# Optimization experiments

Measured on AMD Instinct MI355X. Metric: run time of the kernel, lower is better.

The kernel has to match this reference:

```python
import jax, jax.numpy as jnp
import numpy as np

INF = 1e38  # matches torch source constant


def setup_inputs() -> dict:
    key = jax.random.key(0)
    k1, k2, k3 = jax.random.split(key, 3)
    B, N, D = 16, 2048, 512
    query = jax.random.normal(k1, (B, N, D), dtype=jnp.float32)
    # nn.Linear(dims, dims, bias=False): weight [out, in] = [D, D]
    W_in = jax.random.normal(k2, (D, D), dtype=jnp.float32) * (1.0 / np.sqrt(D))
    # nn.Linear(2*dims, dims, bias=False): weight [D, 2D]
    W_out = jax.random.normal(k3, (D, 2 * D), dtype=jnp.float32) * (1.0 / np.sqrt(2 * D))
    return {"query": query, "W_in": W_in, "W_out": W_out}


def reference(query, W_in, W_out):
    B, N, D = query.shape
    # linear_in: y = x @ W^T
    q = jnp.einsum("bnd,ed->bne", query, W_in)  # [B, N, D]
    # full QK^T scores
    scores = jnp.einsum("bnd,bmd->bnm", q, q)  # [B, N, N]
    # torch: scores[:, triu_mask] = -INF  -> mask upper triangle INCLUDING diagonal
    mask = jnp.triu(jnp.ones((N, N), dtype=bool))
    scores = jnp.where(mask, -INF, scores)
    weights = jax.nn.softmax(scores, axis=-1)
    # row 0 is all -INF -> softmax gives uniform; torch zeroes it explicitly
    weights = weights.at[:, 0, :].set(0.0)
    mix = jnp.einsum("bnm,bmd->bnd", weights, q)  # [B, N, D]
    combined = jnp.concatenate([mix, q], axis=-1)  # [B, N, 2D]
    # linear_out (no activation since activation=None)
    output = jnp.einsum("bnc,dc->bnd", combined, W_out)  # [B, N, D]
    return output
```

## Files before the change

### kernel.cpp

```cpp
#include <hip/hip_runtime.h>

typedef _Float16 f16;
typedef _Float16 half8 __attribute__((ext_vector_type(8)));
typedef _Float16 half4 __attribute__((ext_vector_type(4)));
typedef float floatx4 __attribute__((ext_vector_type(4)));

#define MFMA16(a, b, c) __builtin_amdgcn_mfma_f32_16x16x32_f16(a, b, c, 0, 0, 0)

#define PHASE_WAIT_4()  do { asm volatile("s_waitcnt vmcnt(4)" ::: "memory"); \
    __builtin_amdgcn_sched_barrier(0); __builtin_amdgcn_s_barrier(); } while (0)
#define PHASE_WAIT_0()  do { asm volatile("s_waitcnt vmcnt(0)" ::: "memory"); \
    __builtin_amdgcn_sched_barrier(0); __builtin_amdgcn_s_barrier(); } while (0)

__device__ __forceinline__ void gload16(const void* g, void* l) {
    __builtin_amdgcn_global_load_lds((const __attribute__((address_space(1))) void*)g,
                                     (__attribute__((address_space(3))) void*)l, 16, 0, 0);
}


__global__ __launch_bounds__(256) void k_cvt(const float* __restrict__ query,
                                             const float* __restrict__ Wi,
                                             const float* __restrict__ Wo,
                                             f16* __restrict__ q16,
                                             f16* __restrict__ W16)
{
    int i = blockIdx.x * 256 + threadIdx.x;
    const float4* src;
    f16* dst;
    if (i < 4194304) { src = (const float4*)query + i; dst = q16 + (size_t)i * 4; }
    else if (i < 4259840) { int j = i - 4194304; src = (const float4*)Wi + j; dst = W16 + (size_t)j * 4; }
    else { int j = i - 4259840; src = (const float4*)Wo + j; dst = W16 + 262144 + (size_t)j * 4; }
    float4 v = *src;
    half4 h = {(f16)v.x, (f16)v.y, (f16)v.z, (f16)v.w};
    *reinterpret_cast<half4*>(dst) = h;
}

__global__ __launch_bounds__(512, 4) void k_qin(const f16* __restrict__ q16,
                                                const f16* __restrict__ W16,
                                                f16* __restrict__ comb,
                                                f16* __restrict__ qT)
{
    __shared__ char sm[65536];
    const int tid = threadIdx.x, lane = tid & 63, w = tid >> 6;
    const int l15 = lane & 15, quad = lane >> 4;
    const int id = blockIdx.x, xcd = id & 7, u = id >> 3;
    const int mbase = (xcd * 32 + (u >> 2)) * 128;
    const int nbase = (u & 3) * 128;
    const int wm = (w & 1) * 64, wn = (w >> 1) * 32;
    const int ia = (w & 1) * 4, jb = (w >> 1) * 2;

    floatx4 acc[4][2];
#pragma unroll
    for (int i = 0; i < 4; ++i)
#pragma unroll
        for (int j = 0; j < 2; ++j) acc[i][j] = (floatx4)0.f;

    auto STAGE = [&](int k0, int bsel) {
        f16* At = (f16*)(sm + bsel * 32768);
        f16* Bt = At + 8192;
#pragma unroll
        for (int jr = 0; jr < 2; ++jr) {
            int bi = jr * 8 + w, i2 = bi >> 1, s = bi & 1;
            gload16(q16 + (size_t)(mbase + i2 * 16 + l15) * 512 + k0 + s * 32 + quad * 8, At + bi * 512);
            gload16(W16 + (size_t)(nbase + i2 * 16 + l15) * 512 + k0 + s * 32 + quad * 8, Bt + bi * 512);
        }
    };

    STAGE(0, 0);
    STAGE(64, 1);
    for (int it = 0; it < 8; ++it) {
        const int cur = it & 1;
        if (it < 7) PHASE_WAIT_4(); else PHASE_WAIT_0();
        f16* At = (f16*)(sm + cur * 32768);
        f16* Bt = At + 8192;
#pragma unroll
        for (int s = 0; s < 2; ++s) {
            half8 a[4], bf[2];
#pragma unroll
            for (int i = 0; i < 4; ++i)
                a[i] = *reinterpret_cast<half8*>(At + ((ia + i) * 2 + s) * 512 + lane * 8);
#pragma unroll
            for (int j = 0; j < 2; ++j)
                bf[j] = *reinterpret_cast<half8*>(Bt + ((jb + j) * 2 + s) * 512 + lane * 8);
#pragma unroll
            for (int i = 0; i < 4; ++i)
#pragma unroll
                for (int j = 0; j < 2; ++j)
                    acc[i][j] = MFMA16(a[i], bf[j], acc[i][j]);
        }
        __builtin_amdgcn_s_barrier();
        if (it + 2 < 8) STAGE((it + 2) * 64, cur);
    }
    const int bb = mbase >> 11, tb = mbase & 2047;
    f16* ct = (f16*)sm;
#pragma unroll
    for (int i = 0; i < 4; ++i)
#pragma unroll
        for (int j = 0; j < 2; ++j)
#pragma unroll
            for (int r = 0; r < 4; ++r)
                ct[(wm + i * 16 + quad * 4 + r) * 136 + wn + j * 16 + l15] = (f16)acc[i][j][r];
    __syncthreads();
#pragma unroll
    for (int it = 0; it < 4; ++it) {
        int c = it * 512 + tid, r = c >> 4, c8 = (c & 15) << 3;
        *reinterpret_cast<half8*>(comb + (size_t)(mbase + r) * 1024 + 512 + nbase + c8) =
            *reinterpret_cast<half8*>(ct + r * 136 + c8);
    }
    __syncthreads();
#pragma unroll
    for (int i = 0; i < 4; ++i)
#pragma unroll
        for (int j = 0; j < 2; ++j) {
            half4 h = {(f16)acc[i][j][0], (f16)acc[i][j][1], (f16)acc[i][j][2], (f16)acc[i][j][3]};
            *reinterpret_cast<half4*>(ct + (wn + j * 16 + l15) * 136 + wm + i * 16 + quad * 4) = h;
        }
    __syncthreads();
#pragma unroll
    for (int it = 0; it < 4; ++it) {
        int c = it * 512 + tid, dd = c >> 4, tc = (c & 15) << 3;
        *reinterpret_cast<half8*>(qT + ((size_t)bb * 512 + nbase + dd) * 2048 + tb + tc) =
            *reinterpret_cast<half8*>(ct + dd * 136 + tc);
    }
}

__global__ __launch_bounds__(512, 4) void k_sgemmsm(const f16* __restrict__ comb,
                                                    f16* __restrict__ Pd,
                                                    float* __restrict__ Mt,
                                                    float* __restrict__ Lt)
{
    __shared__ char sm[65536];
    const int tid = threadIdx.x, lane = tid & 63, w = tid >> 6;
    const int l15 = lane & 15, quad = lane >> 4;
    const int wm = (w & 1) * 64, wn = (w >> 1) * 32;
    const int ia = (w & 1) * 4, jb = (w >> 1) * 2;

    const int bhalf = (blockIdx.y >= 136) ? 1 : 0;
    int bx = blockIdx.y - bhalf * 136, mt = 0;
    while ((mt + 1) * (mt + 2) / 2 <= bx) ++mt;
    const int nt = bx - mt * (mt + 1) / 2;
    const int b = blockIdx.x + bhalf * 8;
    const f16* qa = comb + ((size_t)b * 2048 + mt * 128) * 1024 + 512;
    const f16* qb = comb + ((size_t)b * 2048 + nt * 128) * 1024 + 512;

    floatx4 acc[4][2];
#pragma unroll
    for (int i = 0; i < 4; ++i)
#pragma unroll
        for (int j = 0; j < 2; ++j) acc[i][j] = (floatx4)0.f;

    auto STAGE = [&](int k0, int bsel) {
        f16* At = (f16*)(sm + bsel * 32768);
        f16* Bt = At + 8192;
#pragma unroll
        for (int jr = 0; jr < 2; ++jr) {
            int bi = jr * 8 + w, i2 = bi >> 1, s = bi & 1;
            gload16(qa + (size_t)(i2 * 16 + l15) * 1024 + k0 + s * 32 + quad * 8, At + bi * 512);
            gload16(qb + (size_t)(i2 * 16 + l15) * 1024 + k0 + s * 32 + quad * 8, Bt + bi * 512);
        }
    };

    STAGE(0, 0);
    STAGE(64, 1);
    for (int it = 0; it < 8; ++it) {
        const int cur = it & 1;
        if (it < 7) PHASE_WAIT_4(); else PHASE_WAIT_0();
        f16* At = (f16*)(sm + cur * 32768);
        f16* Bt = At + 8192;
#pragma unroll
        for (int s = 0; s < 2; ++s) {
            half8 a[4], bf[2];
#pragma unroll
            for (int i = 0; i < 4; ++i)
                a[i] = *reinterpret_cast<half8*>(At + ((ia + i) * 2 + s) * 512 + lane * 8);
#pragma unroll
            for (int j = 0; j < 2; ++j)
                bf[j] = *reinterpret_cast<half8*>(Bt + ((jb + j) * 2 + s) * 512 + lane * 8);
#pragma unroll
            for (int i = 0; i < 4; ++i)
#pragma unroll
                for (int j = 0; j < 2; ++j)
                    acc[i][j] = MFMA16(a[i], bf[j], acc[i][j]);
        }
        __builtin_amdgcn_s_barrier();
        if (it + 2 < 8) STAGE((it + 2) * 64, cur);
    }

    const bool diag = (nt == mt);
    f16* ct = (f16*)sm;
    float* redm = (float*)(sm + 34816);
    float* reds = (float*)(sm + 36864);
    const int hb = w & 1;

    float wmax[4][4];
#pragma unroll
    for (int i = 0; i < 4; ++i)
#pragma unroll
        for (int r = 0; r < 4; ++r) {
            const int rowl = wm + i * 16 + quad * 4 + r;
            float mm = -1e38f;
#pragma unroll
            for (int j = 0; j < 2; ++j) {
                float v = acc[i][j][r];
                if (diag && (wn + j * 16 + l15) >= rowl) v = -1e38f;
                mm = fmaxf(mm, v);
            }
            mm = fmaxf(mm, __shfl_xor(mm, 1));
            mm = fmaxf(mm, __shfl_xor(mm, 2));
            mm = fmaxf(mm, __shfl_xor(mm, 4));
            mm = fmaxf(mm, __shfl_xor(mm, 8));
            wmax[i][r] = mm;
        }
    if (l15 == 0)
#pragma unroll
        for (int i = 0; i < 4; ++i)
#pragma unroll
            for (int r = 0; r < 4; ++r)
                redm[w * 64 + i * 16 + quad * 4 + r] = wmax[i][r];
    __syncthreads();

#pragma unroll
    for (int i = 0; i < 4; ++i)
#pragma unroll
        for (int r = 0; r < 4; ++r) {
            const int idx = i * 16 + quad * 4 + r;
            const int rowl = wm + idx;
            const float m = fmaxf(fmaxf(redm[hb * 64 + idx], redm[(hb + 2) * 64 + idx]),
                                  fmaxf(redm[(hb + 4) * 64 + idx], redm[(hb + 6) * 64 + idx]));
            float ssum = 0.f;
#pragma unroll
            for (int j = 0; j < 2; ++j) {
                const int col = wn + j * 16 + l15;
                const bool valid = !diag || (col < rowl);
                float e = valid ? __expf(acc[i][j][r] - m) : 0.f;
                ssum += e;
                ct[rowl * 136 + col] = (f16)e;
            }
            ssum += __shfl_xor(ssum, 1);
            ssum += __shfl_xor(ssum, 2);
            ssum += __shfl_xor(ssum, 4);
            ssum += __shfl_xor(ssum, 8);
            wmax[i][r] = ssum;
        }
    if (l15 == 0)
#pragma unroll
        for (int i = 0; i < 4; ++i)
#pragma unroll
            for (int r = 0; r < 4; ++r)
                reds[w * 64 + i * 16 + quad * 4 + r] = wmax[i][r];
    __syncthreads();

    if (tid < 128) {
        const int h2 = tid >> 6, i2 = tid & 63;
        const float mm = fmaxf(fmaxf(redm[h2 * 64 + i2], redm[(h2 + 2) * 64 + i2]),
                               fmaxf(redm[(h2 + 4) * 64 + i2], redm[(h2 + 6) * 64 + i2]));
        const float ll = (reds[h2 * 64 + i2] + reds[(h2 + 2) * 64 + i2])
                       + (reds[(h2 + 4) * 64 + i2] + reds[(h2 + 6) * 64 + i2]);
        const size_t o = (((size_t)b * 16 + nt) << 11) + mt * 128 + tid;
        Mt[o] = mm;
        Lt[o] = ll;
    }
    f16* Pt = Pd + ((size_t)(b * 136 + bx) << 14);
#pragma unroll
    for (int itp = 0; itp < 4; ++itp) {
        int c = itp * 512 + tid, r_ = c >> 4, c8 = (c & 15) << 3;
        *reinterpret_cast<half8*>(Pt + r_ * 128 + c8) =
            *reinterpret_cast<half8*>(ct + r_ * 136 + c8);
    }
}

__global__ __launch_bounds__(256) void k_stats(float* Mt, const float* __restrict__ Lt)
{
    const int b = blockIdx.x, row = blockIdx.y * 256 + threadIdx.x;
    const int mtr = row >> 7;
    float mv[16], lv[16];
    for (int t = 0; t <= mtr; ++t) {
        const size_t o = (((size_t)b * 16 + t) << 11) + row;
        mv[t] = Mt[o];
        lv[t] = Lt[o];
    }
    float M = -1e38f;
    for (int t = 0; t <= mtr; ++t) M = fmaxf(M, mv[t]);
    float l = 0.f;
    for (int t = 0; t <= mtr; ++t) l += lv[t] * __expf(mv[t] - M);
    const float invl = (l > 0.f) ? 1.f / l : 0.f;
    for (int t = 0; t <= mtr; ++t)
        Mt[(((size_t)b * 16 + t) << 11) + row] = __expf(mv[t] - M) * invl;
}

__global__ __launch_bounds__(512, 4) void k_pv(const f16* __restrict__ Pd,
                                               const f16* __restrict__ qT,
                                               f16* __restrict__ comb,
                                               const float* __restrict__ Ft)
{
    extern __shared__ char sm[];
    const int tid = threadIdx.x, lane = tid & 63, w = tid >> 6;
    const int l15 = lane & 15, quad = lane >> 4;
    const int wm = (w & 1) * 64, wn = (w >> 1) * 32;
    const int ia = (w & 1) * 4, jb = (w >> 1) * 2;
    const int id = blockIdx.x;
    const int xcd = id & 7, v = id >> 3;
    const int nb = v & 3, p = (v >> 2) & 7, half_ = v >> 5;
    const int b = xcd + 8 * half_;
    const f16* Pdb = Pd + ((size_t)b * 136 << 14);
    const f16* qTb = qT + ((size_t)b * 512 + nb * 128) * 2048;
    float* F_lds = (float*)(sm + 65536);

    for (int t = 0; t < 2; ++t) {
        const int mt = t ? (15 - p) : p;
        const int tb0 = mt * (mt + 1) / 2;
        const int kit = (mt + 1) * 2;

        if (tid * 4 < (mt + 1) * 128) {
            const int idx = tid * 4, tt = idx >> 7, r4 = idx & 127;
            *reinterpret_cast<floatx4*>(F_lds + idx) =
                *reinterpret_cast<const floatx4*>(Ft + (((size_t)b * 16 + tt) << 11) + mt * 128 + r4);
        }
        __syncthreads();

        floatx4 acc[4][2], accT[4][2];
#pragma unroll
        for (int i = 0; i < 4; ++i)
#pragma unroll
            for (int j = 0; j < 2; ++j) { acc[i][j] = (floatx4)0.f; accT[i][j] = (floatx4)0.f; }

        auto STAGE = [&](int it, int bsel) {
            f16* At = (f16*)(sm + bsel * 32768);
            f16* Bt = At + 8192;
            const int k0 = it * 64;
#pragma unroll
            for (int jr = 0; jr < 2; ++jr) {
                int bi = jr * 8 + w, i2 = bi >> 1, s = bi & 1;
                gload16(Pdb + ((size_t)(tb0 + (k0 >> 7)) << 14) + (size_t)(i2 * 16 + l15) * 128
                            + (k0 & 64) + s * 32 + quad * 8,
                        At + bi * 512);
                gload16(qTb + (size_t)(i2 * 16 + l15) * 2048 + k0 + s * 32 + quad * 8, Bt + bi * 512);
            }
        };

        STAGE(0, 0);
        STAGE(1, 1);
        for (int it = 0; it < kit; ++it) {
            const int cur = it & 1;
            if (it < kit - 1) PHASE_WAIT_4(); else PHASE_WAIT_0();
            f16* At = (f16*)(sm + cur * 32768);
            f16* Bt = At + 8192;
#pragma unroll
            for (int s = 0; s < 2; ++s) {
                half8 a[4], bf[2];
#pragma unroll
                for (int i = 0; i < 4; ++i)
                    a[i] = *reinterpret_cast<half8*>(At + ((ia + i) * 2 + s) * 512 + lane * 8);
#pragma unroll
                for (int j = 0; j < 2; ++j)
                    bf[j] = *reinterpret_cast<half8*>(Bt + ((jb + j) * 2 + s) * 512 + lane * 8);
#pragma unroll
                for (int i = 0; i < 4; ++i)
#pragma unroll
                    for (int j = 0; j < 2; ++j)
                        acc[i][j] = MFMA16(a[i], bf[j], acc[i][j]);
            }
            if (it & 1) {
                const int tt = it >> 1;
                const float* fp = F_lds + tt * 128 + wm;
#pragma unroll
                for (int i = 0; i < 4; ++i) {
                    floatx4 fv = *reinterpret_cast<const floatx4*>(fp + i * 16 + quad * 4);
#pragma unroll
                    for (int j = 0; j < 2; ++j) {
                        accT[i][j] += acc[i][j] * fv;
                        acc[i][j] = (floatx4)0.f;
                    }
                }
            }
            __builtin_amdgcn_s_barrier();
            if (it + 2 < kit) STAGE(it + 2, cur);
        }

        f16* ct = (f16*)sm;
#pragma unroll
        for (int i = 0; i < 4; ++i)
#pragma unroll
            for (int j = 0; j < 2; ++j)
#pragma unroll
                for (int r = 0; r < 4; ++r)
                    ct[(wm + i * 16 + quad * 4 + r) * 136 + wn + j * 16 + l15] = (f16)accT[i][j][r];
        __syncthreads();
#pragma unroll
        for (int it = 0; it < 4; ++it) {
            int c = it * 512 + tid, r = c >> 4, c8 = (c & 15) << 3;
            *reinterpret_cast<half8*>(comb + ((size_t)b * 2048 + mt * 128 + r) * 1024 + nb * 128 + c8) =
                *reinterpret_cast<half8*>(ct + r * 136 + c8);
        }
        __syncthreads();
    }
}

__global__ __launch_bounds__(512, 4) void k_out(const f16* __restrict__ comb,
                                                const f16* __restrict__ Wo16,
                                                float* __restrict__ out)
{
    __shared__ char sm[65536];
    const int tid = threadIdx.x, lane = tid & 63, w = tid >> 6;
    const int l15 = lane & 15, quad = lane >> 4;
    const int id = blockIdx.x, xcd = id & 7, u = id >> 3;
    const int mbase = (xcd * 32 + (u >> 2)) * 128;
    const int nbase = (u & 3) * 128;
    const int wn = (w >> 1) * 32;
    const int ia = (w & 1) * 4, jb = (w >> 1) * 2;

    floatx4 acc[4][2];
#pragma unroll
    for (int i = 0; i < 4; ++i)
#pragma unroll
        for (int j = 0; j < 2; ++j) acc[i][j] = (floatx4)0.f;

    auto STAGE = [&](int k0, int bsel) {
        f16* At = (f16*)(sm + bsel * 32768);
        f16* Bt = At + 8192;
#pragma unroll
        for (int jr = 0; jr < 2; ++jr) {
            int bi = jr * 8 + w, i2 = bi >> 1, s = bi & 1;
            gload16(comb + (size_t)(mbase + i2 * 16 + l15) * 1024 + k0 + s * 32 + quad * 8,
                    At + bi * 512);
            gload16(Wo16 + (size_t)(nbase + i2 * 16 + l15) * 1024 + k0 + s * 32 + quad * 8,
                    Bt + bi * 512);
        }
    };

    STAGE(0, 0);
    STAGE(64, 1);
    for (int it = 0; it < 16; ++it) {
        const int cur = it & 1;
        if (it < 15) PHASE_WAIT_4(); else PHASE_WAIT_0();
        f16* At = (f16*)(sm + cur * 32768);
        f16* Bt = At + 8192;
#pragma unroll
        for (int s = 0; s < 2; ++s) {
            half8 a[4], bf[2];
#pragma unroll
            for (int i = 0; i < 4; ++i)
                a[i] = *reinterpret_cast<half8*>(At + ((ia + i) * 2 + s) * 512 + lane * 8);
#pragma unroll
            for (int j = 0; j < 2; ++j)
                bf[j] = *reinterpret_cast<half8*>(Bt + ((jb + j) * 2 + s) * 512 + lane * 8);
#pragma unroll
            for (int i = 0; i < 4; ++i)
#pragma unroll
                for (int j = 0; j < 2; ++j)
                    acc[i][j] = MFMA16(a[i], bf[j], acc[i][j]);
        }
        __builtin_amdgcn_s_barrier();
        if (it + 2 < 16) STAGE((it + 2) * 64, cur);
    }
    float* cf = (float*)sm;
    for (int pass = 0; pass < 2; ++pass) {
        __syncthreads();
        if ((w & 1) == pass) {
#pragma unroll
            for (int i = 0; i < 4; ++i)
#pragma unroll
                for (int j = 0; j < 2; ++j)
#pragma unroll
                    for (int r = 0; r < 4; ++r)
                        cf[(i * 16 + quad * 4 + r) * 132 + wn + j * 16 + l15] = acc[i][j][r];
        }
        __syncthreads();
#pragma unroll
        for (int it = 0; it < 4; ++it) {
            int c = it * 512 + tid, row = c >> 5, c4 = (c & 31) << 2;
            __builtin_nontemporal_store(
                *reinterpret_cast<floatx4*>(cf + row * 132 + c4),
                reinterpret_cast<floatx4*>(out + (size_t)(mbase + pass * 64 + row) * 512 + nbase + c4));
        }
    }
}

extern "C" void kernel_launch(void* const* d_in, const int* in_sizes, int n_in,
                              void* d_out, int out_size, void* d_ws, size_t ws_size,
                              hipStream_t stream)
{
    const float* query = (const float*)d_in[0];
    const float* W_in  = (const float*)d_in[1];
    const float* W_out = (const float*)d_in[2];
    float* out = (float*)d_out;

    const size_t XOFF = 102236160ull;
    f16* comb = (f16*)d_ws;
    f16* qT   = comb + (size_t)32768 * 1024;
    f16* W16  = qT + (size_t)16 * 512 * 2048;
    f16* q16  = (f16*)((char*)d_ws + XOFF);
    f16* Pd   = (f16*)((char*)d_ws + XOFF);
    float* Mt = (float*)((char*)d_ws + XOFF + 71303168ull);
    float* Lt = (float*)((char*)d_ws + XOFF + 73400320ull);

    k_cvt<<<17152, 256, 0, stream>>>(query, W_in, W_out, q16, W16);
    k_qin<<<1024, 512, 0, stream>>>(q16, W16, comb, qT);
    k_sgemmsm<<<dim3(8, 272), 512, 0, stream>>>(comb, Pd, Mt, Lt);
    k_stats<<<dim3(16, 8), 256, 0, stream>>>(Mt, Lt);
    k_pv<<<512, 512, 73728, stream>>>(Pd, qT, comb, Mt);
    k_out<<<1024, 512, 0, stream>>>(comb, W16 + 262144, out);
}
```

Measured before the change: 373.6 us.

## Enlarge score and output GEMM tiles to 256x256 with dynamic LDS

The score/softmax kernel and the output projection kernel move from 128x128 to 256x256 block tiles. Each wave now holds an 8x4 MFMA accumulator, and large dynamic shared memory buffers replace the fixed static ones. Each 256 score tile is split back into four 128 sub-tiles when writing P and the row stats, and the upper sub-tile of diagonal blocks is skipped. This increases operand reuse and cuts global loads per FLOP, at the cost of fewer blocks (occupancy drops to two per CU and the grid for k_out shrinks to 256 blocks), more register pressure, and wasted compute on the masked diagonal sub-tile.

```diff
diff --git a/kernel.cpp b/kernel.cpp
--- a/kernel.cpp
+++ b/kernel.cpp
@@ -8,6 +8,8 @@
 #define MFMA16(a, b, c) __builtin_amdgcn_mfma_f32_16x16x32_f16(a, b, c, 0, 0, 0)
 
 #define PHASE_WAIT_4()  do { asm volatile("s_waitcnt vmcnt(4)" ::: "memory"); \
+    __builtin_amdgcn_sched_barrier(0); __builtin_amdgcn_s_barrier(); } while (0)
+#define PHASE_WAIT_8()  do { asm volatile("s_waitcnt vmcnt(8)" ::: "memory"); \
     __builtin_amdgcn_sched_barrier(0); __builtin_amdgcn_s_barrier(); } while (0)
 #define PHASE_WAIT_0()  do { asm volatile("s_waitcnt vmcnt(0)" ::: "memory"); \
     __builtin_amdgcn_sched_barrier(0); __builtin_amdgcn_s_barrier(); } while (0)
@@ -124,36 +126,36 @@
     }
 }
 
-__global__ __launch_bounds__(512, 4) void k_sgemmsm(const f16* __restrict__ comb,
+__global__ __launch_bounds__(512, 2) void k_sgemmsm(const f16* __restrict__ comb,
                                                     f16* __restrict__ Pd,
                                                     float* __restrict__ Mt,
                                                     float* __restrict__ Lt)
 {
-    __shared__ char sm[65536];
+    extern __shared__ char sm[];
     const int tid = threadIdx.x, lane = tid & 63, w = tid >> 6;
     const int l15 = lane & 15, quad = lane >> 4;
-    const int wm = (w & 1) * 64, wn = (w >> 1) * 32;
-    const int ia = (w & 1) * 4, jb = (w >> 1) * 2;
-
-    const int bhalf = (blockIdx.y >= 136) ? 1 : 0;
-    int bx = blockIdx.y - bhalf * 136, mt = 0;
-    while ((mt + 1) * (mt + 2) / 2 <= bx) ++mt;
-    const int nt = bx - mt * (mt + 1) / 2;
+    const int rh = w & 1, cq = w >> 1;
+
+    const int bhalf = (blockIdx.y >= 36) ? 1 : 0;
+    int u = blockIdx.y - bhalf * 36, mM = 0;
+    while ((mM + 1) * (mM + 2) / 2 <= u) ++mM;
+    const int nM = u - mM * (mM + 1) / 2;
     const int b = blockIdx.x + bhalf * 8;
-    const f16* qa = comb + ((size_t)b * 2048 + mt * 128) * 1024 + 512;
-    const f16* qb = comb + ((size_t)b * 2048 + nt * 128) * 1024 + 512;
-
-    floatx4 acc[4][2];
-#pragma unroll
-    for (int i = 0; i < 4; ++i)
-#pragma unroll
-        for (int j = 0; j < 2; ++j) acc[i][j] = (floatx4)0.f;
+    const bool diagM = (nM == mM);
+    const f16* qa = comb + ((size_t)b * 2048 + mM * 256) * 1024 + 512;
+    const f16* qb = comb + ((size_t)b * 2048 + nM * 256) * 1024 + 512;
+
+    floatx4 acc[8][4];
+#pragma unroll
+    for (int i = 0; i < 8; ++i)
+#pragma unroll
+        for (int j = 0; j < 4; ++j) acc[i][j] = (floatx4)0.f;
 
     auto STAGE = [&](int k0, int bsel) {
-        f16* At = (f16*)(sm + bsel * 32768);
-        f16* Bt = At + 8192;
-#pragma unroll
-        for (int jr = 0; jr < 2; ++jr) {
+        f16* At = (f16*)sm + bsel * 32768;
+        f16* Bt = At + 16384;
+#pragma unroll
+        for (int jr = 0; jr < 4; ++jr) {
             int bi = jr * 8 + w, i2 = bi >> 1, s = bi & 1;
             gload16(qa + (size_t)(i2 * 16 + l15) * 1024 + k0 + s * 32 + quad * 8, At + bi * 512);
             gload16(qb + (size_t)(i2 * 16 + l15) * 1024 + k0 + s * 32 + quad * 8, Bt + bi * 512);
@@ -164,108 +166,129 @@
     STAGE(64, 1);
     for (int it = 0; it < 8; ++it) {
         const int cur = it & 1;
-        if (it < 7) PHASE_WAIT_4(); else PHASE_WAIT_0();
-        f16* At = (f16*)(sm + cur * 32768);
-        f16* Bt = At + 8192;
+        if (it < 7) PHASE_WAIT_8(); else PHASE_WAIT_0();
+        f16* At = (f16*)sm + cur * 32768;
+        f16* Bt = At + 16384;
 #pragma unroll
         for (int s = 0; s < 2; ++s) {
-            half8 a[4], bf[2];
-#pragma unroll
-            for (int i = 0; i < 4; ++i)
-                a[i] = *reinterpret_cast<half8*>(At + ((ia + i) * 2 + s) * 512 + lane * 8);
-#pragma unroll
-            for (int j = 0; j < 2; ++j)
-                bf[j] = *reinterpret_cast<half8*>(Bt + ((jb + j) * 2 + s) * 512 + lane * 8);
-#pragma unroll
-            for (int i = 0; i < 4; ++i)
-#pragma unroll
-                for (int j = 0; j < 2; ++j)
+            half8 a[8], bf[4];
+#pragma unroll
+            for (int i = 0; i < 8; ++i)
+                a[i] = *reinterpret_cast<half8*>(At + ((rh * 8 + i) * 2 + s) * 512 + lane * 8);
+#pragma unroll
+            for (int j = 0; j < 4; ++j)
+                bf[j] = *reinterpret_cast<half8*>(Bt + ((cq * 4 + j) * 2 + s) * 512 + lane * 8);
+#pragma unroll
+            for (int i = 0; i < 8; ++i)
+#pragma unroll
+                for (int j = 0; j < 4; ++j)
                     acc[i][j] = MFMA16(a[i], bf[j], acc[i][j]);
         }
         __builtin_amdgcn_s_barrier();
         if (it + 2 < 8) STAGE((it + 2) * 64, cur);
     }
 
-    const bool diag = (nt == mt);
-    f16* ct = (f16*)sm;
-    float* redm = (float*)(sm + 34816);
-    float* reds = (float*)(sm + 36864);
-    const int hb = w & 1;
-
-    float wmax[4][4];
-#pragma unroll
-    for (int i = 0; i < 4; ++i)
+    float* redm = (float*)(sm + 135168);
+    float* reds = (float*)(sm + 139264);
+    const int gr0 = mM * 256 + rh * 128;
+    const int gc0 = nM * 256 + cq * 64;
+    const int ch = cq >> 1;
+
+    float st[8][4];
+#pragma unroll
+    for (int i = 0; i < 8; ++i)
 #pragma unroll
         for (int r = 0; r < 4; ++r) {
-            const int rowl = wm + i * 16 + quad * 4 + r;
+            const int rowl = i * 16 + quad * 4 + r;
+            const int gr = gr0 + rowl;
             float mm = -1e38f;
 #pragma unroll
-            for (int j = 0; j < 2; ++j) {
+            for (int j = 0; j < 4; ++j) {
                 float v = acc[i][j][r];
-                if (diag && (wn + j * 16 + l15) >= rowl) v = -1e38f;
+                if (diagM && (gc0 + j * 16 + l15) >= gr) v = -1e38f;
                 mm = fmaxf(mm, v);
             }
             mm = fmaxf(mm, __shfl_xor(mm, 1));
             mm = fmaxf(mm, __shfl_xor(mm, 2));
             mm = fmaxf(mm, __shfl_xor(mm, 4));
             mm = fmaxf(mm, __shfl_xor(mm, 8));
-            wmax[i][r] = mm;
+            st[i][r] = mm;
         }
     if (l15 == 0)
 #pragma unroll
-        for (int i = 0; i < 4; ++i)
+        for (int i = 0; i < 8; ++i)
 #pragma unroll
             for (int r = 0; r < 4; ++r)
-                redm[w * 64 + i * 16 + quad * 4 + r] = wmax[i][r];
+                redm[w * 128 + i * 16 + quad * 4 + r] = st[i][r];
     __syncthreads();
 
 #pragma unroll
-    for (int i = 0; i < 4; ++i)
+    for (int i = 0; i < 8; ++i)
 #pragma unroll
         for (int r = 0; r < 4; ++r) {
-            const int idx = i * 16 + quad * 4 + r;
-            const int rowl = wm + idx;
-            const float m = fmaxf(fmaxf(redm[hb * 64 + idx], redm[(hb + 2) * 64 + idx]),
-                                  fmaxf(redm[(hb + 4) * 64 + idx], redm[(hb + 6) * 64 + idx]));
+            const int rowl = i * 16 + quad * 4 + r;
+            const int gr = gr0 + rowl;
+            const float m = fmaxf(redm[(rh + 4 * ch) * 128 + rowl],
+                                  redm[(rh + 4 * ch + 2) * 128 + rowl]);
             float ssum = 0.f;
 #pragma unroll
-            for (int j = 0; j < 2; ++j) {
-                const int col = wn + j * 16 + l15;
-                const bool valid = !diag || (col < rowl);
+            for (int j = 0; j < 4; ++j) {
+                const bool valid = !diagM || ((gc0 + j * 16 + l15) < gr);
                 float e = valid ? __expf(acc[i][j][r] - m) : 0.f;
                 ssum += e;
-                ct[rowl * 136 + col] = (f16)e;
+                acc[i][j][r] = e;
             }
             ssum += __shfl_xor(ssum, 1);
             ssum += __shfl_xor(ssum, 2);
             ssum += __shfl_xor(ssum, 4);
             ssum += __shfl_xor(ssum, 8);
-            wmax[i][r] = ssum;
+            st[i][r] = ssum;
         }
     if (l15 == 0)
 #pragma unroll
-        for (int i = 0; i < 4; ++i)
+        for (int i = 0; i < 8; ++i)
 #pragma unroll
             for (int r = 0; r < 4; ++r)
-                reds[w * 64 + i * 16 + quad * 4 + r] = wmax[i][r];
+                reds[w * 128 + i * 16 + quad * 4 + r] = st[i][r];
     __syncthreads();
 
-    if (tid < 128) {
-        const int h2 = tid >> 6, i2 = tid & 63;
-        const float mm = fmaxf(fmaxf(redm[h2 * 64 + i2], redm[(h2 + 2) * 64 + i2]),
-                               fmaxf(redm[(h2 + 4) * 64 + i2], redm[(h2 + 6) * 64 + i2]));
-        const float ll = (reds[h2 * 64 + i2] + reds[(h2 + 2) * 64 + i2])
-                       + (reds[(h2 + 4) * 64 + i2] + reds[(h2 + 6) * 64 + i2]);
-        const size_t o = (((size_t)b * 16 + nt) << 11) + mt * 128 + tid;
-        Mt[o] = mm;
-        Lt[o] = ll;
-    }
-    f16* Pt = Pd + ((size_t)(b * 136 + bx) << 14);
-#pragma unroll
-    for (int itp = 0; itp < 4; ++itp) {
-        int c = itp * 512 + tid, r_ = c >> 4, c8 = (c & 15) << 3;
-        *reinterpret_cast<half8*>(Pt + r_ * 128 + c8) =
-            *reinterpret_cast<half8*>(ct + r_ * 136 + c8);
+    {
+        const int row = tid & 127, sub = tid >> 7;
+        const int rh2 = sub & 1, ch2 = sub >> 1;
+        const int mtt = 2 * mM + rh2, nt = 2 * nM + ch2;
+        if (nt <= mtt) {
+            const float mm = fmaxf(redm[(rh2 + 4 * ch2) * 128 + row],
+                                   redm[(rh2 + 4 * ch2 + 2) * 128 + row]);
+            const float ll = reds[(rh2 + 4 * ch2) * 128 + row]
+                           + reds[(rh2 + 4 * ch2 + 2) * 128 + row];
+            const size_t o = (((size_t)b * 16 + nt) << 11) + mtt * 128 + row;
+            Mt[o] = mm;
+            Lt[o] = ll;
+        }
+    }
+
+    f16* ct = (f16*)sm;
+#pragma unroll
+    for (int i = 0; i < 8; ++i)
+#pragma unroll
+        for (int j = 0; j < 4; ++j)
+#pragma unroll
+            for (int r = 0; r < 4; ++r)
+                ct[(rh * 128 + i * 16 + quad * 4 + r) * 260 + cq * 64 + j * 16 + l15] =
+                    (f16)acc[i][j][r];
+    __syncthreads();
+#pragma unroll
+    for (int sub = 0; sub < 4; ++sub) {
+        const int rh2 = sub & 1, ch2 = sub >> 1;
+        const int mtt = 2 * mM + rh2, nt = 2 * nM + ch2;
+        if (nt > mtt) continue;
+        f16* Pt = Pd + ((size_t)(b * 136 + mtt * (mtt + 1) / 2 + nt) << 14);
+#pragma unroll
+        for (int itp = 0; itp < 4; ++itp) {
+            int c = itp * 512 + tid, rr = c >> 4, c8 = (c & 15) << 3;
+            *reinterpret_cast<half8*>(Pt + rr * 128 + c8) =
+                *reinterpret_cast<half8*>(ct + (rh2 * 128 + rr) * 260 + ch2 * 128 + c8);
+        }
     }
 }
 
@@ -396,30 +419,29 @@
     }
 }
 
-__global__ __launch_bounds__(512, 4) void k_out(const f16* __restrict__ comb,
+__global__ __launch_bounds__(512, 2) void k_out(const f16* __restrict__ comb,
                                                 const f16* __restrict__ Wo16,
                                                 float* __restrict__ out)
 {
-    __shared__ char sm[65536];
+    extern __shared__ char sm[];
     const int tid = threadIdx.x, lane = tid & 63, w = tid >> 6;
     const int l15 = lane & 15, quad = lane >> 4;
+    const int rh = w & 1, cq = w >> 1;
     const int id = blockIdx.x, xcd = id & 7, u = id >> 3;
-    const int mbase = (xcd * 32 + (u >> 2)) * 128;
-    const int nbase = (u & 3) * 128;
-    const int wn = (w >> 1) * 32;
-    const int ia = (w & 1) * 4, jb = (w >> 1) * 2;
-
-    floatx4 acc[4][2];
-#pragma unroll
-    for (int i = 0; i < 4; ++i)
-#pragma unroll
-        for (int j = 0; j < 2; ++j) acc[i][j] = (floatx4)0.f;
+    const int mbase = (xcd * 16 + (u >> 1)) * 256;
+    const int nbase = (u & 1) * 256;
+
+    floatx4 acc[8][4];
+#pragma unroll
+    for (int i = 0; i < 8; ++i)
+#pragma unroll
+        for (int j = 0; j < 4; ++j) acc[i][j] = (floatx4)0.f;
 
     auto STAGE = [&](int k0, int bsel) {
-        f16* At = (f16*)(sm + bsel * 32768);
-        f16* Bt = At + 8192;
-#pragma unroll
-        for (int jr = 0; jr < 2; ++jr) {
+        f16* At = (f16*)sm + bsel * 32768;
+        f16* Bt = At + 16384;
+#pragma unroll
+        for (int jr = 0; jr < 4; ++jr) {
             int bi = jr * 8 + w, i2 = bi >> 1, s = bi & 1;
             gload16(comb + (size_t)(mbase + i2 * 16 + l15) * 1024 + k0 + s * 32 + quad * 8,
                     At + bi * 512);
@@ -432,22 +454,22 @@
     STAGE(64, 1);
     for (int it = 0; it < 16; ++it) {
         const int cur = it & 1;
-        if (it < 15) PHASE_WAIT_4(); else PHASE_WAIT_0();
-        f16* At = (f16*)(sm + cur * 32768);
-        f16* Bt = At + 8192;
+        if (it < 15) PHASE_WAIT_8(); else PHASE_WAIT_0();
+        f16* At = (f16*)sm + cur * 32768;
+        f16* Bt = At + 16384;
 #pragma unroll
         for (int s = 0; s < 2; ++s) {
-            half8 a[4], bf[2];
-#pragma unroll
-            for (int i = 0; i < 4; ++i)
-                a[i] = *reinterpret_cast<half8*>(At + ((ia + i) * 2 + s) * 512 + lane * 8);
-#pragma unroll
-            for (int j = 0; j < 2; ++j)
-                bf[j] = *reinterpret_cast<half8*>(Bt + ((jb + j) * 2 + s) * 512 + lane * 8);
-#pragma unroll
-            for (int i = 0; i < 4; ++i)
-#pragma unroll
-                for (int j = 0; j < 2; ++j)
+            half8 a[8], bf[4];
+#pragma unroll
+            for (int i = 0; i < 8; ++i)
+                a[i] = *reinterpret_cast<half8*>(At + ((rh * 8 + i) * 2 + s) * 512 + lane * 8);
+#pragma unroll
+            for (int j = 0; j < 4; ++j)
+                bf[j] = *reinterpret_cast<half8*>(Bt + ((cq * 4 + j) * 2 + s) * 512 + lane * 8);
+#pragma unroll
+            for (int i = 0; i < 8; ++i)
+#pragma unroll
+                for (int j = 0; j < 4; ++j)
                     acc[i][j] = MFMA16(a[i], bf[j], acc[i][j]);
         }
         __builtin_amdgcn_s_barrier();
@@ -456,22 +478,22 @@
     float* cf = (float*)sm;
     for (int pass = 0; pass < 2; ++pass) {
         __syncthreads();
-        if ((w & 1) == pass) {
-#pragma unroll
-            for (int i = 0; i < 4; ++i)
-#pragma unroll
-                for (int j = 0; j < 2; ++j)
+        if (rh == pass) {
+#pragma unroll
+            for (int i = 0; i < 8; ++i)
+#pragma unroll
+                for (int j = 0; j < 4; ++j)
 #pragma unroll
                     for (int r = 0; r < 4; ++r)
-                        cf[(i * 16 + quad * 4 + r) * 132 + wn + j * 16 + l15] = acc[i][j][r];
+                        cf[(i * 16 + quad * 4 + r) * 268 + cq * 64 + j * 16 + l15] = acc[i][j][r];
         }
         __syncthreads();
 #pragma unroll
-        for (int it = 0; it < 4; ++it) {
-            int c = it * 512 + tid, row = c >> 5, c4 = (c & 31) << 2;
+        for (int it = 0; it < 16; ++it) {
+            int c = it * 512 + tid, row = c >> 6, c4 = (c & 63) << 2;
             __builtin_nontemporal_store(
-                *reinterpret_cast<floatx4*>(cf + row * 132 + c4),
-                reinterpret_cast<floatx4*>(out + (size_t)(mbase + pass * 64 + row) * 512 + nbase + c4));
+                *reinterpret_cast<floatx4*>(cf + row * 268 + c4),
+                reinterpret_cast<floatx4*>(out + (size_t)(mbase + pass * 128 + row) * 512 + nbase + c4));
         }
     }
 }
@@ -496,8 +518,8 @@
 
     k_cvt<<<17152, 256, 0, stream>>>(query, W_in, W_out, q16, W16);
     k_qin<<<1024, 512, 0, stream>>>(q16, W16, comb, qT);
-    k_sgemmsm<<<dim3(8, 272), 512, 0, stream>>>(comb, Pd, Mt, Lt);
+    k_sgemmsm<<<dim3(8, 72), 512, 143360, stream>>>(comb, Pd, Mt, Lt);
     k_stats<<<dim3(16, 8), 256, 0, stream>>>(Mt, Lt);
     k_pv<<<512, 512, 73728, stream>>>(Pd, qT, comb, Mt);
-    k_out<<<1024, 512, 0, stream>>>(comb, W16 + 262144, out);
-}
+    k_out<<<256, 512, 139264, stream>>>(comb, W16 + 262144, out);
+}
```

Result: no change. 372.3 us (-0.3%).
